# Optimization experiments

Hardware: AMD Instinct MI355X
Metric: run time of the kernel (lower is better)

The kernel has to match this reference:

```python
import jax, jax.numpy as jnp
import numpy as np

EOS_VALUE = 0
PAD_VALUE = 8192
EPS = 1e-08
B, T, V = 64, 64, 8192  # V == PAD_VALUE by construction of the module


def setup_inputs() -> dict:
    key = jax.random.key(0)
    k1, k2 = jax.random.split(key)
    logits = jax.random.normal(k1, (B, T, V), dtype=jnp.float32)
    targets = jax.random.randint(k2, (B, T), 0, PAD_VALUE + 1, dtype=jnp.int64)
    return {"logits": logits, "targets": targets}


def _knn_cross_entropy(xs, ys, eps):
    # xs: [B, N, D] points in prob space; ys: [B, M, D]
    # distance(i, j) = -sum_d xs[i, d] * log(clip(ys[j, d]))  (all-pairs, then per-i min)
    nb_dim = xs.shape[2]
    soft_ys = jnp.clip(ys, eps, 1.0 - (nb_dim - 1) * eps)
    # [B, N, M] pairwise cross-entropy distances (single big GEMM)
    dist = -jnp.einsum("bnd,bmd->bnm", xs, jnp.log(soft_ys))
    return dist.min(axis=-1).sum()


def reference(logits, targets):
    probs = jax.nn.softmax(logits, axis=-1)              # [B, T, V]
    eos_probs = probs[:, :, EOS_VALUE]                   # [B, T]
    eos_pos = targets == EOS_VALUE
    eos_head = (targets != PAD_VALUE) & (targets != EOS_VALUE)
    eos_target = ~eos_head

    mask = eos_head.astype(probs.dtype)[..., None]       # [B, T, 1]
    probs_m = probs * mask
    # one_hot(num_classes=pad+1), drop last (pad) and first (eos) classes -> [B, T, V-1]
    one_hot = jax.nn.one_hot(targets, PAD_VALUE + 1, dtype=probs.dtype)[:, :, 1:-1] * mask

    xs = probs_m[:, :, 1:]                               # [B, T, V-1]
    label_loss = _knn_cross_entropy(one_hot, xs, EPS) + _knn_cross_entropy(xs, one_hot, EPS)

    # BCELoss(reduction='none') on eos head
    et = eos_target.astype(probs.dtype)
    bce = -(et * jnp.log(eos_probs) + (1.0 - et) * jnp.log(1.0 - eos_probs))  # [B, T]
    ep = eos_pos.astype(probs.dtype)
    eh = eos_head.astype(probs.dtype)
    eos_loss = (
        0.5 * (bce * ep).sum(axis=1) / (ep.sum(axis=1) + EPS)
        + 0.5 * (bce * eh).sum(axis=1) / (eh.sum(axis=1) + EPS)
    ).mean()

    return label_loss, eos_loss
```

## Files before the change

kernel.cpp:

```cpp
#include <hip/hip_runtime.h>
#include <math.h>

#define B_ 64
#define T_ 64
#define V_ 8192

#define L0_ (-18.420680743952367f)
#define L1_ (-8.190335e-05f)
#define HI_ (0.99991810f)
#define EPS_ (1e-8f)

#define OFF_T2 262144
#define OFF_BA 266240
#define OFF_BH 270336

__device__ __forceinline__ float waveReduceMax(float v) {
    #pragma unroll
    for (int off = 32; off; off >>= 1) v = fmaxf(v, __shfl_xor(v, off));
    return v;
}
__device__ __forceinline__ float waveReduceSum(float v) {
    #pragma unroll
    for (int off = 32; off; off >>= 1) v += __shfl_xor(v, off);
    return v;
}

__global__ __launch_bounds__(256) void k_row(const float* __restrict__ logits,
                                             const int* __restrict__ targets,
                                             float* __restrict__ wsf,
                                             float* __restrict__ out) {
    const int row = blockIdx.x;
    const int b   = row >> 6;
    const int n   = row & 63;
    const int tid = threadIdx.x;
    if (row == 0 && tid < 2) out[tid] = 0.0f;

    const float4* rp4 = (const float4*)(logits + (size_t)row * V_);

    float s = 0.0f;
    #pragma unroll
    for (int k = 0; k < 8; ++k) {
        const float4 t = rp4[tid + (k << 8)];
        s += __expf(t.x) + __expf(t.y) + __expf(t.z) + __expf(t.w);
    }
    s = waveReduceSum(s);

    const int lane = tid & 63, wid = tid >> 6;
    __shared__ float ss[4];
    if (lane == 0) ss[wid] = s;
    __syncthreads();

    if (tid >= 64) return;
    const float Z  = ss[0] + ss[1] + ss[2] + ss[3];
    const float iZ = 1.0f / Z;
    const float p0 = __expf(logits[(size_t)row * V_]) * iZ;

    const int  j      = tid;
    const int  tj     = targets[b * 64 + j];
    const bool headj  = (tj != 0) && (tj != 8192);
    const int  tn     = __shfl(tj, n);
    const bool head_n = (tn != 0) && (tn != 8192);
    const bool isz_n  = (tn == 0);

    float pj = 0.0f;
    if (head_n && headj)
        pj = __expf(logits[(size_t)row * V_ + tj]) * iZ;
    wsf[(size_t)row * 64 + j] = pj;

    const float rm = waveReduceMax(pj);
    if (j == 0) {
        wsf[OFF_T2 + row] = head_n ? ((-L0_) * (1.0f - p0) - (L1_ - L0_) * rm) : 0.0f;
        wsf[OFF_BA + row] = isz_n  ? -__logf(p0)        : 0.0f;
        wsf[OFF_BH + row] = head_n ? -__logf(1.0f - p0) : 0.0f;
    }
}

__global__ __launch_bounds__(256) void k_batch(const int* __restrict__ targets,
                                               const float* __restrict__ wsf,
                                               float* __restrict__ out) {
    const int b   = blockIdx.x;
    const int tid = threadIdx.x;
    const int j   = tid & 63, g = tid >> 6;

    const float* Pb = wsf + (size_t)b * 64 * 64;
    float cm = 0.0f;
    #pragma unroll
    for (int nn = 0; nn < 16; ++nn)
        cm = fmaxf(cm, Pb[(g * 16 + nn) * 64 + j]);

    __shared__ float scm[256];
    scm[tid] = cm;
    __syncthreads();

    if (tid >= 64) return;
    const float cmj = fmaxf(fmaxf(scm[j], scm[64 + j]),
                            fmaxf(scm[128 + j], scm[192 + j]));
    const int  tj    = targets[b * 64 + j];
    const bool headj = (tj != 0) && (tj != 8192);

    float t1 = headj ? -__logf(fminf(fmaxf(cmj, EPS_), HI_)) : 0.0f;
    float lab = t1 + wsf[OFF_T2 + b * 64 + j];
    float a   = wsf[OFF_BA + b * 64 + j];
    float h   = wsf[OFF_BH + b * 64 + j];
    float cz  = (tj == 0) ? 1.0f : 0.0f;
    float ch  = headj     ? 1.0f : 0.0f;

    lab = waveReduceSum(lab);
    a   = waveReduceSum(a);
    h   = waveReduceSum(h);
    cz  = waveReduceSum(cz);
    ch  = waveReduceSum(ch);
    if (tid == 0) {
        atomicAdd(&out[0], lab);
        atomicAdd(&out[1], (0.5f * a / (cz + EPS_) + 0.5f * h / (ch + EPS_)) * (1.0f / 64.0f));
    }
}

extern "C" void kernel_launch(void* const* d_in, const int* in_sizes, int n_in,
                              void* d_out, int out_size, void* d_ws, size_t ws_size,
                              hipStream_t stream) {
    const float* logits  = (const float*)d_in[0];
    const int*   targets = (const int*)d_in[1];
    float* out = (float*)d_out;
    float* wsf = (float*)d_ws;

    k_row<<<dim3(B_ * T_), dim3(256), 0, stream>>>(logits, targets, wsf, out);
    k_batch<<<dim3(B_), dim3(256), 0, stream>>>(targets, wsf, out);
}
```

Before: 31.90 us.

## Assign one wavefront per row in k_row, dropping shared-memory block reduction

Each 256-thread block now processes four rows, one per wavefront, instead of one row per block. Each wave sums its full 8192-element row with four independent accumulators, so the row sum needs only a wave shuffle reduction, with no LDS exchange and no __syncthreads. All four waves stay busy in the epilogue instead of three exiting early. The trade-off is fewer blocks and more serial loads per lane, which relies on memory-level parallelism from the unrolled loads to keep HBM bandwidth saturated.

```diff
diff --git a/kernel.cpp b/kernel.cpp
--- a/kernel.cpp
+++ b/kernel.cpp
@@ -29,33 +29,34 @@
                                              const int* __restrict__ targets,
                                              float* __restrict__ wsf,
                                              float* __restrict__ out) {
-    const int row = blockIdx.x;
-    const int b   = row >> 6;
-    const int n   = row & 63;
-    const int tid = threadIdx.x;
-    if (row == 0 && tid < 2) out[tid] = 0.0f;
+    const int tid  = threadIdx.x;
+    const int wid  = tid >> 6;
+    const int lane = tid & 63;
+    const int row  = (blockIdx.x << 2) + wid;
+    const int b    = row >> 6;
+    const int n    = row & 63;
+    if (row == 0 && lane < 2) out[lane] = 0.0f;
 
     const float4* rp4 = (const float4*)(logits + (size_t)row * V_);
 
-    float s = 0.0f;
+    float s0 = 0.0f, s1 = 0.0f, s2 = 0.0f, s3 = 0.0f;
     #pragma unroll
     for (int k = 0; k < 8; ++k) {
-        const float4 t = rp4[tid + (k << 8)];
-        s += __expf(t.x) + __expf(t.y) + __expf(t.z) + __expf(t.w);
+        const float4 a = rp4[lane + ((k * 4 + 0) << 6)];
+        const float4 c = rp4[lane + ((k * 4 + 1) << 6)];
+        const float4 d = rp4[lane + ((k * 4 + 2) << 6)];
+        const float4 e = rp4[lane + ((k * 4 + 3) << 6)];
+        s0 += __expf(a.x) + __expf(a.y) + __expf(a.z) + __expf(a.w);
+        s1 += __expf(c.x) + __expf(c.y) + __expf(c.z) + __expf(c.w);
+        s2 += __expf(d.x) + __expf(d.y) + __expf(d.z) + __expf(d.w);
+        s3 += __expf(e.x) + __expf(e.y) + __expf(e.z) + __expf(e.w);
     }
-    s = waveReduceSum(s);
+    const float Z = waveReduceSum((s0 + s1) + (s2 + s3));
 
-    const int lane = tid & 63, wid = tid >> 6;
-    __shared__ float ss[4];
-    if (lane == 0) ss[wid] = s;
-    __syncthreads();
-
-    if (tid >= 64) return;
-    const float Z  = ss[0] + ss[1] + ss[2] + ss[3];
     const float iZ = 1.0f / Z;
     const float p0 = __expf(logits[(size_t)row * V_]) * iZ;
 
-    const int  j      = tid;
+    const int  j      = lane;
     const int  tj     = targets[b * 64 + j];
     const bool headj  = (tj != 0) && (tj != 8192);
     const int  tn     = __shfl(tj, n);
@@ -124,6 +125,6 @@
     float* out = (float*)d_out;
     float* wsf = (float*)d_ws;
 
-    k_row<<<dim3(B_ * T_), dim3(256), 0, stream>>>(logits, targets, wsf, out);
+    k_row<<<dim3(B_ * T_ / 4), dim3(256), 0, stream>>>(logits, targets, wsf, out);
     k_batch<<<dim3(B_), dim3(256), 0, stream>>>(targets, wsf, out);
 }
```

Result: faster. 31.27 us (-2.0%).
